# Optimization experiments

Hardware: AMD Instinct MI355X
Metric: run time of the kernel (lower is better)

Reference implementation:

```python
import jax, jax.numpy as jnp
import numpy as np

ALPHA_1 = 0.5
ALPHA_2 = 0.9
TAU = 0.1
BIG_NUM = 1.0e9


def setup_inputs() -> dict:
    key = jax.random.key(0)
    k1, k2 = jax.random.split(key)
    B, N_SUP, N_QRY, D = 4, 512, 4096, 128
    features = jax.random.normal(k1, (B, N_SUP + N_QRY, D), dtype=jnp.float32)
    support_labels = jax.random.randint(k2, (B, N_SUP), 0, 64, dtype=jnp.int64)
    return {"features": features, "support_labels": support_labels}


def _sq_dists(x, y):
    # squared Euclidean pairwise distances: [B, N, M]
    xn = jnp.sum(x * x, axis=-1)  # [B, N]
    yn = jnp.sum(y * y, axis=-1)  # [B, M]
    xy = jnp.einsum('bnd,bmd->bnm', x, y)
    return xn[:, :, None] + yn[:, None, :] - 2.0 * xy


def reference(features, support_labels):
    n_support = support_labels.shape[1]
    support = features[:, :n_support]   # [B, S, D]
    query = features[:, n_support:]     # [B, Q, D]

    # --- re_represent_queries ---
    logits = -TAU * _sq_dists(query, query)           # [B, Q, Q]
    Q = query.shape[1]
    rng = jnp.arange(Q)
    logits = logits.at[:, rng, rng].set(-BIG_NUM)     # mask self-similarity
    attn_q = jax.nn.softmax(logits, axis=2)
    # Faithful to source: (attn[:,:,:,None] * q[:,:,None,:]).sum(2)
    # i.e. row index of q matches row index of attn; softmax axis j is contracted
    # against a broadcast copy of the same row.
    re_rep_q = jnp.einsum('bij,bid->bid', attn_q, query)
    new_query = (1.0 - ALPHA_1) * query + ALPHA_1 * re_rep_q

    # --- re_represent_supports ---
    logits_s = -TAU * _sq_dists(support, new_query)   # [B, S, Q]
    attn_s = jax.nn.softmax(logits_s, axis=2)
    re_rep_s = jnp.einsum('bsq,bqd->bsd', attn_s, new_query)
    new_support = (1.0 - ALPHA_2) * support + ALPHA_2 * re_rep_s

    return jnp.concatenate((new_support, new_query), axis=1)
```

## Files before the change

### kernel.cpp

```cpp
#include <hip/hip_runtime.h>

#define BATCH 4
#define NS 512
#define NQ 4096
#define D 128
#define NTOT (NS + NQ)

#define NCHUNK 16
#define QCHUNK (NQ / NCHUNK)
#define QT 64
#define ST 128
#define PITN 136
#define PITT 72

typedef __attribute__((ext_vector_type(8))) short bf16x8;
typedef __attribute__((ext_vector_type(4))) float f32x4;

#define L2E 1.4426950408889634f
#define SCL 0.28853900817779268f

__device__ __forceinline__ unsigned short f2bf(float f) {
    unsigned int x = __float_as_uint(f);
    return (unsigned short)((x + 0x7fffu + ((x >> 16) & 1u)) >> 16);
}

__global__ __launch_bounds__(256) void attend_kernel(const float* __restrict__ feat,
                                                     float* __restrict__ out,
                                                     float* __restrict__ accP,
                                                     float* __restrict__ lsumP) {
    __shared__ unsigned short qn_[QT * PITN];
    __shared__ unsigned short qt_[D * PITT];
    __shared__ unsigned short p_[ST * PITT];
    __shared__ float qns[QCHUNK];

    int chunk = blockIdx.x, stile = blockIdx.y, b = blockIdx.z;
    int s0 = stile * ST;
    int q0 = chunk * QCHUNK;
    int t = threadIdx.x;
    int w = t >> 6, ln = t & 15, quad = (t >> 4) & 3;

    bf16x8 asup[2][4];
    #pragma unroll
    for (int mt = 0; mt < 2; ++mt) {
        const float* srow = feat + ((size_t)b * NTOT + s0 + 64 * mt + 16 * w + ln) * D;
        #pragma unroll
        for (int kk = 0; kk < 4; ++kk) {
            float4 lo = *(const float4*)(srow + 32 * kk + 8 * quad);
            float4 hi = *(const float4*)(srow + 32 * kk + 8 * quad + 4);
            union { bf16x8 v; unsigned short u[8]; } pk;
            pk.u[0] = f2bf(lo.x); pk.u[1] = f2bf(lo.y); pk.u[2] = f2bf(lo.z); pk.u[3] = f2bf(lo.w);
            pk.u[4] = f2bf(hi.x); pk.u[5] = f2bf(hi.y); pk.u[6] = f2bf(hi.z); pk.u[7] = f2bf(hi.w);
            asup[mt][kk] = pk.v;
        }
    }

    f32x4 cpv[2][8];
    #pragma unroll
    for (int mt = 0; mt < 2; ++mt)
        #pragma unroll
        for (int ds = 0; ds < 8; ++ds) cpv[mt][ds] = (f32x4){0.f, 0.f, 0.f, 0.f};
    float lpart[2][4] = {{0.f,0.f,0.f,0.f},{0.f,0.f,0.f,0.f}};

    int qrow = t >> 2;
    int dgrp = (t & 3) * 4;
    const float* qchunk_base = feat + ((size_t)b * NTOT + NS + q0) * D;
    float* outq = out + ((size_t)b * NTOT + NS + q0) * D;
    int copy_qt = stile * QT;

    for (int qt = 0; qt < QCHUNK; qt += QT) {
        __syncthreads();
        const float* qbase = qchunk_base + (size_t)(qt + qrow) * D;
        float nrm = 0.f;
        int docopy = (qt == copy_qt);
        #pragma unroll
        for (int i = 0; i < 8; ++i) {
            int d = dgrp + 16 * i;
            float4 v = *(const float4*)(qbase + d);
            if (docopy) *(float4*)(outq + (size_t)(qt + qrow) * D + d) = v;
            nrm += v.x * v.x + v.y * v.y + v.z * v.z + v.w * v.w;
            unsigned short b0 = f2bf(v.x), b1 = f2bf(v.y), b2 = f2bf(v.z), b3 = f2bf(v.w);
            *(unsigned int*)&qn_[qrow * PITN + d]     = (unsigned)b0 | ((unsigned)b1 << 16);
            *(unsigned int*)&qn_[qrow * PITN + d + 2] = (unsigned)b2 | ((unsigned)b3 << 16);
            qt_[(d + 0) * PITT + qrow] = b0;
            qt_[(d + 1) * PITT + qrow] = b1;
            qt_[(d + 2) * PITT + qrow] = b2;
            qt_[(d + 3) * PITT + qrow] = b3;
        }
        nrm += __shfl_xor(nrm, 1, 64);
        nrm += __shfl_xor(nrm, 2, 64);
        if ((t & 3) == 0) qns[qt + qrow] = 0.1f * L2E * nrm;
        __syncthreads();

        f32x4 cqk[2][4];
        #pragma unroll
        for (int mt = 0; mt < 2; ++mt)
            #pragma unroll
            for (int f = 0; f < 4; ++f) cqk[mt][f] = (f32x4){0.f, 0.f, 0.f, 0.f};
        #pragma unroll
        for (int kk = 0; kk < 4; ++kk) {
            #pragma unroll
            for (int f = 0; f < 4; ++f) {
                bf16x8 bq = *(const bf16x8*)&qn_[(16 * f + ln) * PITN + 32 * kk + 8 * quad];
                #pragma unroll
                for (int mt = 0; mt < 2; ++mt)
                    cqk[mt][f] = __builtin_amdgcn_mfma_f32_16x16x32_bf16(asup[mt][kk], bq,
                                                                         cqk[mt][f], 0, 0, 0);
            }
        }

        #pragma unroll
        for (int mt = 0; mt < 2; ++mt)
            #pragma unroll
            for (int f = 0; f < 4; ++f) {
                float qs = qns[qt + 16 * f + ln];
                #pragma unroll
                for (int r = 0; r < 4; ++r) {
                    float e = exp2f(SCL * cqk[mt][f][r] - qs);
                    lpart[mt][r] += e;
                    p_[(64 * mt + 16 * w + 4 * quad + r) * PITT + 16 * f + ln] = f2bf(e);
                }
            }
        __syncthreads();

        #pragma unroll
        for (int kk = 0; kk < 2; ++kk) {
            bf16x8 ap[2];
            #pragma unroll
            for (int mt = 0; mt < 2; ++mt)
                ap[mt] = *(const bf16x8*)&p_[(64 * mt + 16 * w + ln) * PITT + 32 * kk + 8 * quad];
            #pragma unroll
            for (int ds = 0; ds < 8; ++ds) {
                bf16x8 bv = *(const bf16x8*)&qt_[(16 * ds + ln) * PITT + 32 * kk + 8 * quad];
                #pragma unroll
                for (int mt = 0; mt < 2; ++mt)
                    cpv[mt][ds] = __builtin_amdgcn_mfma_f32_16x16x32_bf16(ap[mt], bv,
                                                                          cpv[mt][ds], 0, 0, 0);
            }
        }
    }

    int base = (chunk * BATCH + b) * NS + s0;
    #pragma unroll
    for (int mt = 0; mt < 2; ++mt)
        #pragma unroll
        for (int r = 0; r < 4; ++r) {
            float v = lpart[mt][r];
            v += __shfl_xor(v, 1, 64);
            v += __shfl_xor(v, 2, 64);
            v += __shfl_xor(v, 4, 64);
            v += __shfl_xor(v, 8, 64);
            if (ln == 0) lsumP[base + 64 * mt + 16 * w + 4 * quad + r] = v;
        }
    #pragma unroll
    for (int mt = 0; mt < 2; ++mt)
        #pragma unroll
        for (int ds = 0; ds < 8; ++ds)
            #pragma unroll
            for (int r = 0; r < 4; ++r)
                accP[(size_t)(base + 64 * mt + 16 * w + 4 * quad + r) * D + 16 * ds + ln] =
                    cpv[mt][ds][r];
}

__global__ __launch_bounds__(256) void epi_kernel(const float* __restrict__ feat,
                                                  const float* __restrict__ accP,
                                                  const float* __restrict__ lsumP,
                                                  float* __restrict__ out) {
    int wave = threadIdx.x >> 6;
    int lane = threadIdx.x & 63;
    int row = blockIdx.x * 4 + wave;
    int b = row >> 9;
    int s = row & (NS - 1);

    float l = 0.f, ax = 0.f, ay = 0.f;
    #pragma unroll 4
    for (int c = 0; c < NCHUNK; ++c) {
        int base = (c * BATCH + b) * NS + s;
        l += lsumP[base];
        float2 a = *(const float2*)(accP + (size_t)base * D + lane * 2);
        ax += a.x; ay += a.y;
    }
    float inv = 0.9f / l;
    size_t fo = ((size_t)b * NTOT + s) * D + lane * 2;
    float2 sup = *(const float2*)(feat + fo);
    float2 o;
    o.x = 0.1f * sup.x + ax * inv;
    o.y = 0.1f * sup.y + ay * inv;
    *(float2*)(out + fo) = o;
}

extern "C" void kernel_launch(void* const* d_in, const int* in_sizes, int n_in,
                              void* d_out, int out_size, void* d_ws, size_t ws_size,
                              hipStream_t stream) {
    const float* feat = (const float*)d_in[0];
    float* out = (float*)d_out;
    float* ws = (float*)d_ws;
    float* accP  = ws;
    float* lsumP = accP + (size_t)NCHUNK * BATCH * NS * D;
    (void)in_sizes; (void)n_in; (void)out_size; (void)ws_size;

    attend_kernel<<<dim3(NCHUNK, NS / ST, BATCH), 256, 0, stream>>>(feat, out, accP, lsumP);
    epi_kernel<<<BATCH * NS / 4, 256, 0, stream>>>(feat, accP, lsumP, out);
}
```

Measured before the change: 88.56 us.

## Double query chunks, pack bf16 conversions, and drop redundant barrier

Splits the query dimension into 32 chunks instead of 16, which doubles the block count so more CUs have work, and sets launch bounds to allow two blocks per CU. The query pass-through copy is split by row halves so each query row is still written exactly once. Float-to-bf16 conversion now goes through a packed two-value builtin when it exists. The barrier before the P·V MFMA is removed because each wave reads only the P rows it wrote itself. In exchange, the partial accumulator buffer and the epilogue reduction become twice as large, adding global memory traffic.

```diff
diff --git a/kernel.cpp b/kernel.cpp
--- a/kernel.cpp
+++ b/kernel.cpp
@@ -6,7 +6,7 @@
 #define D 128
 #define NTOT (NS + NQ)
 
-#define NCHUNK 16
+#define NCHUNK 32
 #define QCHUNK (NQ / NCHUNK)
 #define QT 64
 #define ST 128
@@ -24,10 +24,20 @@
     return (unsigned short)((x + 0x7fffu + ((x >> 16) & 1u)) >> 16);
 }
 
-__global__ __launch_bounds__(256) void attend_kernel(const float* __restrict__ feat,
-                                                     float* __restrict__ out,
-                                                     float* __restrict__ accP,
-                                                     float* __restrict__ lsumP) {
+__device__ __forceinline__ unsigned int pk2(float a, float b) {
+#if __has_builtin(__builtin_amdgcn_cvt_pk_bf16_f32)
+    typedef __bf16 bf2 __attribute__((ext_vector_type(2)));
+    bf2 r = __builtin_amdgcn_cvt_pk_bf16_f32(a, b);
+    return __builtin_bit_cast(unsigned int, r);
+#else
+    return (unsigned)f2bf(a) | ((unsigned)f2bf(b) << 16);
+#endif
+}
+
+__global__ __launch_bounds__(256, 2) void attend_kernel(const float* __restrict__ feat,
+                                                        float* __restrict__ out,
+                                                        float* __restrict__ accP,
+                                                        float* __restrict__ lsumP) {
     __shared__ unsigned short qn_[QT * PITN];
     __shared__ unsigned short qt_[D * PITT];
     __shared__ unsigned short p_[ST * PITT];
@@ -47,9 +57,11 @@
         for (int kk = 0; kk < 4; ++kk) {
             float4 lo = *(const float4*)(srow + 32 * kk + 8 * quad);
             float4 hi = *(const float4*)(srow + 32 * kk + 8 * quad + 4);
-            union { bf16x8 v; unsigned short u[8]; } pk;
-            pk.u[0] = f2bf(lo.x); pk.u[1] = f2bf(lo.y); pk.u[2] = f2bf(lo.z); pk.u[3] = f2bf(lo.w);
-            pk.u[4] = f2bf(hi.x); pk.u[5] = f2bf(hi.y); pk.u[6] = f2bf(hi.z); pk.u[7] = f2bf(hi.w);
+            union { bf16x8 v; unsigned int u[4]; } pk;
+            pk.u[0] = pk2(lo.x, lo.y);
+            pk.u[1] = pk2(lo.z, lo.w);
+            pk.u[2] = pk2(hi.x, hi.y);
+            pk.u[3] = pk2(hi.z, hi.w);
             asup[mt][kk] = pk.v;
         }
     }
@@ -65,26 +77,27 @@
     int dgrp = (t & 3) * 4;
     const float* qchunk_base = feat + ((size_t)b * NTOT + NS + q0) * D;
     float* outq = out + ((size_t)b * NTOT + NS + q0) * D;
-    int copy_qt = stile * QT;
+    int copy_qt = (stile >> 1) << 6;
+    int copy_ok = (qrow >> 5) == (stile & 1);
 
     for (int qt = 0; qt < QCHUNK; qt += QT) {
         __syncthreads();
         const float* qbase = qchunk_base + (size_t)(qt + qrow) * D;
         float nrm = 0.f;
-        int docopy = (qt == copy_qt);
+        int docopy = (qt == copy_qt) & copy_ok;
         #pragma unroll
         for (int i = 0; i < 8; ++i) {
             int d = dgrp + 16 * i;
             float4 v = *(const float4*)(qbase + d);
             if (docopy) *(float4*)(outq + (size_t)(qt + qrow) * D + d) = v;
             nrm += v.x * v.x + v.y * v.y + v.z * v.z + v.w * v.w;
-            unsigned short b0 = f2bf(v.x), b1 = f2bf(v.y), b2 = f2bf(v.z), b3 = f2bf(v.w);
-            *(unsigned int*)&qn_[qrow * PITN + d]     = (unsigned)b0 | ((unsigned)b1 << 16);
-            *(unsigned int*)&qn_[qrow * PITN + d + 2] = (unsigned)b2 | ((unsigned)b3 << 16);
-            qt_[(d + 0) * PITT + qrow] = b0;
-            qt_[(d + 1) * PITT + qrow] = b1;
-            qt_[(d + 2) * PITT + qrow] = b2;
-            qt_[(d + 3) * PITT + qrow] = b3;
+            unsigned int p01 = pk2(v.x, v.y);
+            unsigned int p23 = pk2(v.z, v.w);
+            *(uint2*)&qn_[qrow * PITN + d] = make_uint2(p01, p23);
+            qt_[(d + 0) * PITT + qrow] = (unsigned short)p01;
+            qt_[(d + 1) * PITT + qrow] = (unsigned short)(p01 >> 16);
+            qt_[(d + 2) * PITT + qrow] = (unsigned short)p23;
+            qt_[(d + 3) * PITT + qrow] = (unsigned short)(p23 >> 16);
         }
         nrm += __shfl_xor(nrm, 1, 64);
         nrm += __shfl_xor(nrm, 2, 64);
@@ -114,13 +127,18 @@
             for (int f = 0; f < 4; ++f) {
                 float qs = qns[qt + 16 * f + ln];
                 #pragma unroll
-                for (int r = 0; r < 4; ++r) {
-                    float e = exp2f(SCL * cqk[mt][f][r] - qs);
-                    lpart[mt][r] += e;
-                    p_[(64 * mt + 16 * w + 4 * quad + r) * PITT + 16 * f + ln] = f2bf(e);
+                for (int r = 0; r < 4; r += 2) {
+                    float e0 = exp2f(SCL * cqk[mt][f][r]     - qs);
+                    float e1 = exp2f(SCL * cqk[mt][f][r + 1] - qs);
+                    lpart[mt][r] += e0;
+                    lpart[mt][r + 1] += e1;
+                    unsigned int pe = pk2(e0, e1);
+                    p_[(64 * mt + 16 * w + 4 * quad + r)     * PITT + 16 * f + ln] =
+                        (unsigned short)pe;
+                    p_[(64 * mt + 16 * w + 4 * quad + r + 1) * PITT + 16 * f + ln] =
+                        (unsigned short)(pe >> 16);
                 }
             }
-        __syncthreads();
 
         #pragma unroll
         for (int kk = 0; kk < 2; ++kk) {
```

New measurement: 86.70 us. 2.1% less time.
